# Kernel tuning notes

Hardware: AMD Instinct MI355X
Metric: run time of the kernel (lower is better)

The kernel has to match this reference:

```python
import jax, jax.numpy as jnp
import numpy as np

H = 64  # hidden size (fixed by module)

def _gru_cell(x, h, Wih, Whh, bih, bhh):
    # PyTorch GRU cell: gates ordered (r, z, n)
    gi = x @ Wih.T + bih            # [B, 3H]
    gh = h @ Whh.T + bhh            # [B, 3H]
    ir, iz, inn = jnp.split(gi, 3, axis=-1)
    hr, hz, hn = jnp.split(gh, 3, axis=-1)
    r = jax.nn.sigmoid(ir + hr)
    z = jax.nn.sigmoid(iz + hz)
    n = jnp.tanh(inn + r * hn)
    return (1.0 - z) * n + z * h


def setup_inputs() -> dict:
    key = jax.random.key(0)
    ks = jax.random.split(key, 24)
    B, T, NI = 16384, 256, 6
    s = 1.0 / np.sqrt(H)  # torch default GRU init scale
    f32 = jnp.float32
    u = lambda k, shp: jax.random.uniform(k, shp, dtype=f32, minval=-s, maxval=s)
    inp = {
        "x": jax.random.normal(ks[0], (B, T, NI), dtype=f32),
        "target_len": 180,
        # encoder GRU, layer 0 (input size NI) and layer 1 (input size H)
        "e_Wih0": u(ks[1], (3 * H, NI)), "e_Whh0": u(ks[2], (3 * H, H)),
        "e_bih0": u(ks[3], (3 * H,)),    "e_bhh0": u(ks[4], (3 * H,)),
        "e_Wih1": u(ks[5], (3 * H, H)),  "e_Whh1": u(ks[6], (3 * H, H)),
        "e_bih1": u(ks[7], (3 * H,)),    "e_bhh1": u(ks[8], (3 * H,)),
        # decoder GRU, layer 0 (input size 1) and layer 1 (input size H)
        "d_Wih0": u(ks[9], (3 * H, 1)),  "d_Whh0": u(ks[10], (3 * H, H)),
        "d_bih0": u(ks[11], (3 * H,)),   "d_bhh0": u(ks[12], (3 * H,)),
        "d_Wih1": u(ks[13], (3 * H, H)), "d_Whh1": u(ks[14], (3 * H, H)),
        "d_bih1": u(ks[15], (3 * H,)),   "d_bhh1": u(ks[16], (3 * H,)),
        # heads
        "W_on": u(ks[17], (1, H)), "b_on": u(ks[18], (1,)),
        "W_cv": u(ks[19], (1, H)), "b_cv": u(ks[20], (1,)),
    }
    return inp


def reference(x, target_len,
              e_Wih0, e_Whh0, e_bih0, e_bhh0, e_Wih1, e_Whh1, e_bih1, e_bhh1,
              d_Wih0, d_Whh0, d_bih0, d_bhh0, d_Wih1, d_Whh1, d_bih1, d_bhh1,
              W_on, b_on, W_cv, b_cv):
    B = x.shape[0]
    on_threshold = 0.5

    # ---- encoder: 2-layer GRU over the input sequence, keep final hidden ----
    def enc_step(carry, xt):
        h0, h1 = carry
        h0 = _gru_cell(xt, h0, e_Wih0, e_Whh0, e_bih0, e_bhh0)
        h1 = _gru_cell(h0, h1, e_Wih1, e_Whh1, e_bih1, e_bhh1)
        return (h0, h1), None

    h_init = (jnp.zeros((B, H), x.dtype), jnp.zeros((B, H), x.dtype))
    (h0, h1), _ = jax.lax.scan(enc_step, h_init, jnp.swapaxes(x, 0, 1))  # [T,B,NI]

    def dec_step(carry, _):
        prev, h0, h1 = carry                                   # prev: [B,1]
        h0 = _gru_cell(prev, h0, d_Wih0, d_Whh0, d_bih0, d_bhh0)
        h1 = _gru_cell(h0, h1, d_Wih1, d_Whh1, d_bih1, d_bhh1)
        cv = h1 @ W_cv.T + b_cv                                # [B,1]
        logit = h1 @ W_on.T + b_on                             # [B,1]
        gated = (jax.nn.sigmoid(logit) > on_threshold).astype(cv.dtype) * cv
        return (gated, h0, h1), gated

    prev0 = jnp.zeros((B, 1), x.dtype)
    _, outs = jax.lax.scan(dec_step, (prev0, h0, h1), None, length=target_len)
    # outs: [target_len, B, 1] -> [B, target_len, 1] (torch.cat along dim=1)
    return jnp.swapaxes(outs, 0, 1)
```

## Files before the change

kernel.cpp:

```cpp
#include <hip/hip_runtime.h>
#include <math.h>

#define TENC 256
#define NIE  6
#define LH   68
#define WSTR 68

__shared__ float sW1[192 * WSTR];
__shared__ float sU1[192 * WSTR];
__shared__ float sHd[132];
__shared__ float sh0[64 * LH];
__shared__ float sh1[64 * LH];

__device__ __forceinline__ float sigm_(float x) { return 1.0f / (1.0f + expf(-x)); }

__device__ __forceinline__ void fma4(float& acc, const float4& a, const float4& b) {
    acc = fmaf(a.x, b.x, acc);
    acc = fmaf(a.y, b.y, acc);
    acc = fmaf(a.z, b.z, acc);
    acc = fmaf(a.w, b.w, acc);
}

__device__ __forceinline__ void stage_w1(const float* __restrict__ W1,
                                         const float* __restrict__ U1) {
    for (int s = threadIdx.x; s < 12288; s += 512) {
        int k = s & 63, row = s >> 6;
        int g = row >> 6, j = row & 63;
        int d = (j * 3 + g) * WSTR + k;
        sW1[d] = W1[s];
        sU1[d] = U1[s];
    }
}

template<int KIN>
__device__ __forceinline__ void layer0_c(const float* __restrict__ U0,
                                         const float* w0r, const float* w0z,
                                         const float* w0n,
                                         const float* xin,
                                         const float* b_r, const float* b_z,
                                         const float* b_nx, const float* b_nh,
                                         int jB, int bl, float hn[2][4])
{
    float ar[2][4], az[2][4], anx[2][4], anh[2][4];
#pragma unroll
    for (int g = 0; g < 4; ++g) {
#pragma unroll
        for (int jj = 0; jj < 2; ++jj) {
            ar[jj][g] = b_r[jj]; az[jj][g] = b_z[jj];
            anx[jj][g] = b_nx[jj]; anh[jj][g] = b_nh[jj];
        }
    }
#pragma unroll
    for (int jj = 0; jj < 2; ++jj)
#pragma unroll
        for (int g = 0; g < 4; ++g)
#pragma unroll
            for (int k = 0; k < KIN; ++k) {
                ar[jj][g]  = fmaf(w0r[jj * KIN + k], xin[g * KIN + k], ar[jj][g]);
                az[jj][g]  = fmaf(w0z[jj * KIN + k], xin[g * KIN + k], az[jj][g]);
                anx[jj][g] = fmaf(w0n[jj * KIN + k], xin[g * KIN + k], anx[jj][g]);
            }
    const float* u0 = U0 + (size_t)jB * 64;
    const float* u1 = U0 + (size_t)(jB + 1) * 64;
    const float* hr0 = sh0 + bl * LH;
#pragma unroll 2
    for (int kc = 0; kc < 64; kc += 4) {
        float4 hv[4];
#pragma unroll
        for (int g = 0; g < 4; ++g)
            hv[g] = *(const float4*)(hr0 + g * (16 * LH) + kc);
        float4 r0 = *(const float4*)(u0 + kc);
        float4 z0 = *(const float4*)(u0 + 4096 + kc);
        float4 n0 = *(const float4*)(u0 + 8192 + kc);
        float4 r1 = *(const float4*)(u1 + kc);
        float4 z1 = *(const float4*)(u1 + 4096 + kc);
        float4 n1 = *(const float4*)(u1 + 8192 + kc);
#pragma unroll
        for (int g = 0; g < 4; ++g) {
            fma4(ar[0][g], r0, hv[g]); fma4(az[0][g], z0, hv[g]); fma4(anh[0][g], n0, hv[g]);
            fma4(ar[1][g], r1, hv[g]); fma4(az[1][g], z1, hv[g]); fma4(anh[1][g], n1, hv[g]);
        }
    }
#pragma unroll
    for (int g = 0; g < 4; ++g) {
        float2 ho = *(const float2*)(sh0 + (bl + 16 * g) * LH + jB);
        float hold[2] = {ho.x, ho.y};
#pragma unroll
        for (int jj = 0; jj < 2; ++jj) {
            float r = sigm_(ar[jj][g]);
            float z = sigm_(az[jj][g]);
            float n = tanhf(fmaf(r, anh[jj][g], anx[jj][g]));
            hn[jj][g] = fmaf(z, hold[jj] - n, n);
        }
    }
}

__device__ __forceinline__ void layer1_c(const float* b_r, const float* b_z,
                                         const float* b_nx, const float* b_nh,
                                         int jB, int bl, float hn[2][4])
{
    float ar[2][4], az[2][4], anx[2][4], anh[2][4];
#pragma unroll
    for (int g = 0; g < 4; ++g) {
#pragma unroll
        for (int jj = 0; jj < 2; ++jj) {
            ar[jj][g] = b_r[jj]; az[jj][g] = b_z[jj];
            anx[jj][g] = b_nx[jj]; anh[jj][g] = b_nh[jj];
        }
    }
    const float* wb0 = sW1 + (jB * 3) * WSTR;
    const float* wb1 = sW1 + ((jB + 1) * 3) * WSTR;
    const float* ub0 = sU1 + (jB * 3) * WSTR;
    const float* ub1 = sU1 + ((jB + 1) * 3) * WSTR;
    const float* xr0 = sh0 + bl * LH;
    const float* hr0 = sh1 + bl * LH;
#pragma unroll 2
    for (int kc = 0; kc < 64; kc += 4) {
        float4 xv[4], hv[4];
#pragma unroll
        for (int g = 0; g < 4; ++g) {
            xv[g] = *(const float4*)(xr0 + g * (16 * LH) + kc);
            hv[g] = *(const float4*)(hr0 + g * (16 * LH) + kc);
        }
        float4 wr0 = *(const float4*)(wb0 + kc);
        float4 wz0 = *(const float4*)(wb0 + WSTR + kc);
        float4 wn0 = *(const float4*)(wb0 + 2 * WSTR + kc);
        float4 ur0 = *(const float4*)(ub0 + kc);
        float4 uz0 = *(const float4*)(ub0 + WSTR + kc);
        float4 un0 = *(const float4*)(ub0 + 2 * WSTR + kc);
        float4 wr1 = *(const float4*)(wb1 + kc);
        float4 wz1 = *(const float4*)(wb1 + WSTR + kc);
        float4 wn1 = *(const float4*)(wb1 + 2 * WSTR + kc);
        float4 ur1 = *(const float4*)(ub1 + kc);
        float4 uz1 = *(const float4*)(ub1 + WSTR + kc);
        float4 un1 = *(const float4*)(ub1 + 2 * WSTR + kc);
#pragma unroll
        for (int g = 0; g < 4; ++g) {
            fma4(ar[0][g], wr0, xv[g]);  fma4(ar[0][g], ur0, hv[g]);
            fma4(az[0][g], wz0, xv[g]);  fma4(az[0][g], uz0, hv[g]);
            fma4(anx[0][g], wn0, xv[g]); fma4(anh[0][g], un0, hv[g]);
            fma4(ar[1][g], wr1, xv[g]);  fma4(ar[1][g], ur1, hv[g]);
            fma4(az[1][g], wz1, xv[g]);  fma4(az[1][g], uz1, hv[g]);
            fma4(anx[1][g], wn1, xv[g]); fma4(anh[1][g], un1, hv[g]);
        }
    }
#pragma unroll
    for (int g = 0; g < 4; ++g) {
        float2 ho = *(const float2*)(sh1 + (bl + 16 * g) * LH + jB);
        float hold[2] = {ho.x, ho.y};
#pragma unroll
        for (int jj = 0; jj < 2; ++jj) {
            float r = sigm_(ar[jj][g]);
            float z = sigm_(az[jj][g]);
            float n = tanhf(fmaf(r, anh[jj][g], anx[jj][g]));
            hn[jj][g] = fmaf(z, hold[jj] - n, n);
        }
    }
}

extern "C" __global__ void __launch_bounds__(512, 2)
ccseq_kernel(const float* __restrict__ x, const int* __restrict__ p_tlen,
             const float* __restrict__ eW0, const float* __restrict__ eU0,
             const float* __restrict__ eBi0, const float* __restrict__ eBh0,
             const float* __restrict__ eW1, const float* __restrict__ eU1,
             const float* __restrict__ eBi1, const float* __restrict__ eBh1,
             const float* __restrict__ dW0, const float* __restrict__ dU0,
             const float* __restrict__ dBi0, const float* __restrict__ dBh0,
             const float* __restrict__ dW1, const float* __restrict__ dU1,
             const float* __restrict__ dBi1, const float* __restrict__ dBh1,
             const float* __restrict__ Won, const float* __restrict__ bon,
             const float* __restrict__ Wcv, const float* __restrict__ bcv,
             float* __restrict__ out)
{
    const int tid  = threadIdx.x;
    const int lane = tid & 63;
    const int wv   = tid >> 6;
    const int jg   = lane >> 4;
    const int bl   = lane & 15;
    const int jB   = wv * 8 + jg * 2;
    const int tlen = p_tlen[0];

    if (tid < 64) { sHd[tid] = Wcv[tid]; sHd[64 + tid] = Won[tid]; }
    for (int i = tid; i < 64 * LH; i += 512) { sh0[i] = 0.0f; sh1[i] = 0.0f; }
    stage_w1(eW1, eU1);
    __syncthreads();

    float w0r[2 * NIE], w0z[2 * NIE], w0n[2 * NIE];
#pragma unroll
    for (int jj = 0; jj < 2; ++jj)
#pragma unroll
        for (int k = 0; k < NIE; ++k) {
            w0r[jj * NIE + k] = eW0[(jB + jj) * NIE + k];
            w0z[jj * NIE + k] = eW0[(64 + jB + jj) * NIE + k];
            w0n[jj * NIE + k] = eW0[(128 + jB + jj) * NIE + k];
        }
    float eb_r[2], eb_z[2], eb_nx[2], eb_nh[2];
    float e1_r[2], e1_z[2], e1_nx[2], e1_nh[2];
#pragma unroll
    for (int jj = 0; jj < 2; ++jj) {
        int j = jB + jj;
        eb_r[jj]  = eBi0[j] + eBh0[j];
        eb_z[jj]  = eBi0[64 + j] + eBh0[64 + j];
        eb_nx[jj] = eBi0[128 + j];
        eb_nh[jj] = eBh0[128 + j];
        e1_r[jj]  = eBi1[j] + eBh1[j];
        e1_z[jj]  = eBi1[64 + j] + eBh1[64 + j];
        e1_nx[jj] = eBi1[128 + j];
        e1_nh[jj] = eBh1[128 + j];
    }

    const size_t bstr = (size_t)TENC * NIE;
    const float* xb[4];
#pragma unroll
    for (int g = 0; g < 4; ++g)
        xb[g] = x + (size_t)(blockIdx.x * 64 + bl + 16 * g) * bstr;

    float xc[4 * NIE], xn[4 * NIE];
#pragma unroll
    for (int g = 0; g < 4; ++g)
#pragma unroll
        for (int k = 0; k < NIE; ++k) xc[g * NIE + k] = xb[g][k];

    for (int t = 0; t < TENC; ++t) {
        const int tn = (t + 1 < TENC) ? (t + 1) : t;
#pragma unroll
        for (int g = 0; g < 4; ++g)
#pragma unroll
            for (int k = 0; k < NIE; ++k) xn[g * NIE + k] = xb[g][tn * NIE + k];

        float hn[2][4];
        layer0_c<NIE>(eU0, w0r, w0z, w0n, xc, eb_r, eb_z, eb_nx, eb_nh, jB, bl, hn);
        __syncthreads();
#pragma unroll
        for (int g = 0; g < 4; ++g)
            *(float2*)(sh0 + (bl + 16 * g) * LH + jB) = make_float2(hn[0][g], hn[1][g]);
        __syncthreads();

        layer1_c(e1_r, e1_z, e1_nx, e1_nh, jB, bl, hn);
        __syncthreads();
#pragma unroll
        for (int g = 0; g < 4; ++g)
            *(float2*)(sh1 + (bl + 16 * g) * LH + jB) = make_float2(hn[0][g], hn[1][g]);
        __syncthreads();

#pragma unroll
        for (int i = 0; i < 4 * NIE; ++i) xc[i] = xn[i];
    }

    stage_w1(dW1, dU1);
    float v0r[2], v0z[2], v0n[2];
    float db_r[2], db_z[2], db_nx[2], db_nh[2];
    float d1_r[2], d1_z[2], d1_nx[2], d1_nh[2];
#pragma unroll
    for (int jj = 0; jj < 2; ++jj) {
        int j = jB + jj;
        v0r[jj] = dW0[j]; v0z[jj] = dW0[64 + j]; v0n[jj] = dW0[128 + j];
        db_r[jj]  = dBi0[j] + dBh0[j];
        db_z[jj]  = dBi0[64 + j] + dBh0[64 + j];
        db_nx[jj] = dBi0[128 + j];
        db_nh[jj] = dBh0[128 + j];
        d1_r[jj]  = dBi1[j] + dBh1[j];
        d1_z[jj]  = dBi1[64 + j] + dBh1[64 + j];
        d1_nx[jj] = dBi1[128 + j];
        d1_nh[jj] = dBh1[128 + j];
    }
    const float hbc = bcv[0], hbo = bon[0];
    __syncthreads();

    float prev[4] = {0.0f, 0.0f, 0.0f, 0.0f};
    for (int t = 0; t < tlen; ++t) {
        float hn[2][4];
        layer0_c<1>(dU0, v0r, v0z, v0n, prev, db_r, db_z, db_nx, db_nh, jB, bl, hn);
        __syncthreads();
#pragma unroll
        for (int g = 0; g < 4; ++g)
            *(float2*)(sh0 + (bl + 16 * g) * LH + jB) = make_float2(hn[0][g], hn[1][g]);
        __syncthreads();

        layer1_c(d1_r, d1_z, d1_nx, d1_nh, jB, bl, hn);
        __syncthreads();
#pragma unroll
        for (int g = 0; g < 4; ++g)
            *(float2*)(sh1 + (bl + 16 * g) * LH + jB) = make_float2(hn[0][g], hn[1][g]);
        __syncthreads();

        float cv[4] = {hbc, hbc, hbc, hbc};
        float lg[4] = {hbo, hbo, hbo, hbo};
        const float* hr0 = sh1 + bl * LH;
#pragma unroll 2
        for (int kc = 0; kc < 64; kc += 4) {
            float4 wc = *(const float4*)(sHd + kc);
            float4 wo = *(const float4*)(sHd + 64 + kc);
#pragma unroll
            for (int g = 0; g < 4; ++g) {
                float4 h4 = *(const float4*)(hr0 + g * (16 * LH) + kc);
                fma4(cv[g], wc, h4);
                fma4(lg[g], wo, h4);
            }
        }
#pragma unroll
        for (int g = 0; g < 4; ++g)
            prev[g] = (lg[g] > 0.0f) ? cv[g] : 0.0f;
        if (tid < 16) {
#pragma unroll
            for (int g = 0; g < 4; ++g)
                out[(size_t)(blockIdx.x * 64 + bl + 16 * g) * tlen + t] = prev[g];
        }
    }
}

extern "C" void kernel_launch(void* const* d_in, const int* in_sizes, int n_in,
                              void* d_out, int out_size, void* d_ws, size_t ws_size,
                              hipStream_t stream)
{
    (void)n_in; (void)out_size; (void)d_ws; (void)ws_size;
    const float* x    = (const float*)d_in[0];
    const int*   tl   = (const int*)d_in[1];
    const float* eW0  = (const float*)d_in[2];
    const float* eU0  = (const float*)d_in[3];
    const float* eBi0 = (const float*)d_in[4];
    const float* eBh0 = (const float*)d_in[5];
    const float* eW1  = (const float*)d_in[6];
    const float* eU1  = (const float*)d_in[7];
    const float* eBi1 = (const float*)d_in[8];
    const float* eBh1 = (const float*)d_in[9];
    const float* dW0  = (const float*)d_in[10];
    const float* dU0  = (const float*)d_in[11];
    const float* dBi0 = (const float*)d_in[12];
    const float* dBh0 = (const float*)d_in[13];
    const float* dW1  = (const float*)d_in[14];
    const float* dU1  = (const float*)d_in[15];
    const float* dBi1 = (const float*)d_in[16];
    const float* dBh1 = (const float*)d_in[17];
    const float* Won  = (const float*)d_in[18];
    const float* bon  = (const float*)d_in[19];
    const float* Wcv  = (const float*)d_in[20];
    const float* bcv  = (const float*)d_in[21];

    const int B    = in_sizes[0] / (TENC * NIE);
    const int nblk = B / 64;

    ccseq_kernel<<<dim3(nblk), dim3(512), 0, stream>>>(
        x, tl, eW0, eU0, eBi0, eBh0, eW1, eU1, eBi1, eBh1,
        dW0, dU0, dBi0, dBh0, dW1, dU1, dBi1, dBh1,
        Won, bon, Wcv, bcv, (float*)d_out);
}
```

Measured before the change: 9.694 ms.

## Double-buffer hidden states to halve barriers and read W1 from global

Hidden states are ping-ponged between two LDS buffers per layer, so new values are written straight to the other buffer and each layer update needs one barrier instead of two. The layer-1 input weights are read from global memory (cache) instead of LDS, which frees shared memory for the extra buffers. Encoder input loads are also vectorized into float2 reads. The trade-off is more global/cache weight traffic in the inner layer-1 loop and more LDS spent on buffers.

New measurement: 10.26 ms. 1.06x slower.

```diff
diff --git a/kernel.cpp b/kernel.cpp
--- a/kernel.cpp
+++ b/kernel.cpp
@@ -6,11 +6,10 @@
 #define LH   68
 #define WSTR 68
 
-__shared__ float sW1[192 * WSTR];
 __shared__ float sU1[192 * WSTR];
 __shared__ float sHd[132];
-__shared__ float sh0[64 * LH];
-__shared__ float sh1[64 * LH];
+__shared__ float sh0a[64 * LH], sh0b[64 * LH];
+__shared__ float sh1a[64 * LH], sh1b[64 * LH];
 
 __device__ __forceinline__ float sigm_(float x) { return 1.0f / (1.0f + expf(-x)); }
 
@@ -21,14 +20,11 @@
     acc = fmaf(a.w, b.w, acc);
 }
 
-__device__ __forceinline__ void stage_w1(const float* __restrict__ W1,
-                                         const float* __restrict__ U1) {
+__device__ __forceinline__ void stage_u1(const float* __restrict__ U1) {
     for (int s = threadIdx.x; s < 12288; s += 512) {
         int k = s & 63, row = s >> 6;
         int g = row >> 6, j = row & 63;
-        int d = (j * 3 + g) * WSTR + k;
-        sW1[d] = W1[s];
-        sU1[d] = U1[s];
+        sU1[(j * 3 + g) * WSTR + k] = U1[s];
     }
 }
 
@@ -39,17 +35,17 @@
                                          const float* xin,
                                          const float* b_r, const float* b_z,
                                          const float* b_nx, const float* b_nh,
+                                         const float* __restrict__ h0r,
                                          int jB, int bl, float hn[2][4])
 {
     float ar[2][4], az[2][4], anx[2][4], anh[2][4];
 #pragma unroll
-    for (int g = 0; g < 4; ++g) {
+    for (int g = 0; g < 4; ++g)
 #pragma unroll
         for (int jj = 0; jj < 2; ++jj) {
             ar[jj][g] = b_r[jj]; az[jj][g] = b_z[jj];
             anx[jj][g] = b_nx[jj]; anh[jj][g] = b_nh[jj];
         }
-    }
 #pragma unroll
     for (int jj = 0; jj < 2; ++jj)
 #pragma unroll
@@ -62,7 +58,7 @@
             }
     const float* u0 = U0 + (size_t)jB * 64;
     const float* u1 = U0 + (size_t)(jB + 1) * 64;
-    const float* hr0 = sh0 + bl * LH;
+    const float* hr0 = h0r + bl * LH;
 #pragma unroll 2
     for (int kc = 0; kc < 64; kc += 4) {
         float4 hv[4];
@@ -83,7 +79,7 @@
     }
 #pragma unroll
     for (int g = 0; g < 4; ++g) {
-        float2 ho = *(const float2*)(sh0 + (bl + 16 * g) * LH + jB);
+        float2 ho = *(const float2*)(h0r + (bl + 16 * g) * LH + jB);
         float hold[2] = {ho.x, ho.y};
 #pragma unroll
         for (int jj = 0; jj < 2; ++jj) {
@@ -95,42 +91,43 @@
     }
 }
 
-__device__ __forceinline__ void layer1_c(const float* b_r, const float* b_z,
+__device__ __forceinline__ void layer1_c(const float* __restrict__ W1,
+                                         const float* b_r, const float* b_z,
                                          const float* b_nx, const float* b_nh,
+                                         const float* __restrict__ x0r,
+                                         const float* __restrict__ h1r,
                                          int jB, int bl, float hn[2][4])
 {
     float ar[2][4], az[2][4], anx[2][4], anh[2][4];
 #pragma unroll
-    for (int g = 0; g < 4; ++g) {
+    for (int g = 0; g < 4; ++g)
 #pragma unroll
         for (int jj = 0; jj < 2; ++jj) {
             ar[jj][g] = b_r[jj]; az[jj][g] = b_z[jj];
             anx[jj][g] = b_nx[jj]; anh[jj][g] = b_nh[jj];
         }
-    }
-    const float* wb0 = sW1 + (jB * 3) * WSTR;
-    const float* wb1 = sW1 + ((jB + 1) * 3) * WSTR;
+    const float* wp = W1 + (size_t)jB * 64;
     const float* ub0 = sU1 + (jB * 3) * WSTR;
     const float* ub1 = sU1 + ((jB + 1) * 3) * WSTR;
-    const float* xr0 = sh0 + bl * LH;
-    const float* hr0 = sh1 + bl * LH;
+    const float* xr0 = x0r + bl * LH;
+    const float* hr0 = h1r + bl * LH;
 #pragma unroll 2
     for (int kc = 0; kc < 64; kc += 4) {
+        float4 wr0 = *(const float4*)(wp + kc);
+        float4 wz0 = *(const float4*)(wp + 4096 + kc);
+        float4 wn0 = *(const float4*)(wp + 8192 + kc);
+        float4 wr1 = *(const float4*)(wp + 64 + kc);
+        float4 wz1 = *(const float4*)(wp + 4160 + kc);
+        float4 wn1 = *(const float4*)(wp + 8256 + kc);
         float4 xv[4], hv[4];
 #pragma unroll
         for (int g = 0; g < 4; ++g) {
             xv[g] = *(const float4*)(xr0 + g * (16 * LH) + kc);
             hv[g] = *(const float4*)(hr0 + g * (16 * LH) + kc);
         }
-        float4 wr0 = *(const float4*)(wb0 + kc);
-        float4 wz0 = *(const float4*)(wb0 + WSTR + kc);
-        float4 wn0 = *(const float4*)(wb0 + 2 * WSTR + kc);
         float4 ur0 = *(const float4*)(ub0 + kc);
         float4 uz0 = *(const float4*)(ub0 + WSTR + kc);
         float4 un0 = *(const float4*)(ub0 + 2 * WSTR + kc);
-        float4 wr1 = *(const float4*)(wb1 + kc);
-        float4 wz1 = *(const float4*)(wb1 + WSTR + kc);
-        float4 wn1 = *(const float4*)(wb1 + 2 * WSTR + kc);
         float4 ur1 = *(const float4*)(ub1 + kc);
         float4 uz1 = *(const float4*)(ub1 + WSTR + kc);
         float4 un1 = *(const float4*)(ub1 + 2 * WSTR + kc);
@@ -146,7 +143,7 @@
     }
 #pragma unroll
     for (int g = 0; g < 4; ++g) {
-        float2 ho = *(const float2*)(sh1 + (bl + 16 * g) * LH + jB);
+        float2 ho = *(const float2*)(h1r + (bl + 16 * g) * LH + jB);
         float hold[2] = {ho.x, ho.y};
 #pragma unroll
         for (int jj = 0; jj < 2; ++jj) {
@@ -181,9 +178,14 @@
     const int tlen = p_tlen[0];
 
     if (tid < 64) { sHd[tid] = Wcv[tid]; sHd[64 + tid] = Won[tid]; }
-    for (int i = tid; i < 64 * LH; i += 512) { sh0[i] = 0.0f; sh1[i] = 0.0f; }
-    stage_w1(eW1, eU1);
+    for (int i = tid; i < 64 * LH; i += 512) {
+        sh0a[i] = 0.0f; sh0b[i] = 0.0f; sh1a[i] = 0.0f; sh1b[i] = 0.0f;
+    }
+    stage_u1(eU1);
     __syncthreads();
+
+    float* r0 = sh0a; float* w0 = sh0b;
+    float* r1 = sh1a; float* w1 = sh1b;
 
     float w0r[2 * NIE], w0z[2 * NIE], w0n[2 * NIE];
 #pragma unroll
@@ -217,37 +219,47 @@
 
     float xc[4 * NIE], xn[4 * NIE];
 #pragma unroll
-    for (int g = 0; g < 4; ++g)
-#pragma unroll
-        for (int k = 0; k < NIE; ++k) xc[g * NIE + k] = xb[g][k];
+    for (int g = 0; g < 4; ++g) {
+        float2 p0 = *(const float2*)(xb[g]);
+        float2 p1 = *(const float2*)(xb[g] + 2);
+        float2 p2 = *(const float2*)(xb[g] + 4);
+        xc[g * NIE + 0] = p0.x; xc[g * NIE + 1] = p0.y;
+        xc[g * NIE + 2] = p1.x; xc[g * NIE + 3] = p1.y;
+        xc[g * NIE + 4] = p2.x; xc[g * NIE + 5] = p2.y;
+    }
 
     for (int t = 0; t < TENC; ++t) {
         const int tn = (t + 1 < TENC) ? (t + 1) : t;
 #pragma unroll
-        for (int g = 0; g < 4; ++g)
-#pragma unroll
-            for (int k = 0; k < NIE; ++k) xn[g * NIE + k] = xb[g][tn * NIE + k];
+        for (int g = 0; g < 4; ++g) {
+            float2 p0 = *(const float2*)(xb[g] + tn * NIE);
+            float2 p1 = *(const float2*)(xb[g] + tn * NIE + 2);
+            float2 p2 = *(const float2*)(xb[g] + tn * NIE + 4);
+            xn[g * NIE + 0] = p0.x; xn[g * NIE + 1] = p0.y;
+            xn[g * NIE + 2] = p1.x; xn[g * NIE + 3] = p1.y;
+            xn[g * NIE + 4] = p2.x; xn[g * NIE + 5] = p2.y;
+        }
 
         float hn[2][4];
-        layer0_c<NIE>(eU0, w0r, w0z, w0n, xc, eb_r, eb_z, eb_nx, eb_nh, jB, bl, hn);
+        layer0_c<NIE>(eU0, w0r, w0z, w0n, xc, eb_r, eb_z, eb_nx, eb_nh, r0, jB, bl, hn);
+#pragma unroll
+        for (int g = 0; g < 4; ++g)
+            *(float2*)(w0 + (bl + 16 * g) * LH + jB) = make_float2(hn[0][g], hn[1][g]);
         __syncthreads();
-#pragma unroll
-        for (int g = 0; g < 4; ++g)
-            *(float2*)(sh0 + (bl + 16 * g) * LH + jB) = make_float2(hn[0][g], hn[1][g]);
+
+        layer1_c(eW1, e1_r, e1_z, e1_nx, e1_nh, w0, r1, jB, bl, hn);
+#pragma unroll
+        for (int g = 0; g < 4; ++g)
+            *(float2*)(w1 + (bl + 16 * g) * LH + jB) = make_float2(hn[0][g], hn[1][g]);
         __syncthreads();
 
-        layer1_c(e1_r, e1_z, e1_nx, e1_nh, jB, bl, hn);
-        __syncthreads();
-#pragma unroll
-        for (int g = 0; g < 4; ++g)
-            *(float2*)(sh1 + (bl + 16 * g) * LH + jB) = make_float2(hn[0][g], hn[1][g]);
-        __syncthreads();
-
+        { float* tp = r0; r0 = w0; w0 = tp; }
+        { float* tp = r1; r1 = w1; w1 = tp; }
 #pragma unroll
         for (int i = 0; i < 4 * NIE; ++i) xc[i] = xn[i];
     }
 
-    stage_w1(dW1, dU1);
+    stage_u1(dU1);
     float v0r[2], v0z[2], v0n[2];
     float db_r[2], db_z[2], db_nx[2], db_nh[2];
     float d1_r[2], d1_z[2], d1_nx[2], d1_nh[2];
@@ -270,23 +282,21 @@
     float prev[4] = {0.0f, 0.0f, 0.0f, 0.0f};
     for (int t = 0; t < tlen; ++t) {
         float hn[2][4];
-        layer0_c<1>(dU0, v0r, v0z, v0n, prev, db_r, db_z, db_nx, db_nh, jB, bl, hn);
+        layer0_c<1>(dU0, v0r, v0z, v0n, prev, db_r, db_z, db_nx, db_nh, r0, jB, bl, hn);
+#pragma unroll
+        for (int g = 0; g < 4; ++g)
+            *(float2*)(w0 + (bl + 16 * g) * LH + jB) = make_float2(hn[0][g], hn[1][g]);
         __syncthreads();
-#pragma unroll
-        for (int g = 0; g < 4; ++g)
-            *(float2*)(sh0 + (bl + 16 * g) * LH + jB) = make_float2(hn[0][g], hn[1][g]);
-        __syncthreads();
-
-        layer1_c(d1_r, d1_z, d1_nx, d1_nh, jB, bl, hn);
-        __syncthreads();
-#pragma unroll
-        for (int g = 0; g < 4; ++g)
-            *(float2*)(sh1 + (bl + 16 * g) * LH + jB) = make_float2(hn[0][g], hn[1][g]);
+
+        layer1_c(dW1, d1_r, d1_z, d1_nx, d1_nh, w0, r1, jB, bl, hn);
+#pragma unroll
+        for (int g = 0; g < 4; ++g)
+            *(float2*)(w1 + (bl + 16 * g) * LH + jB) = make_float2(hn[0][g], hn[1][g]);
         __syncthreads();
 
         float cv[4] = {hbc, hbc, hbc, hbc};
         float lg[4] = {hbo, hbo, hbo, hbo};
-        const float* hr0 = sh1 + bl * LH;
+        const float* hr0 = w1 + bl * LH;
 #pragma unroll 2
         for (int kc = 0; kc < 64; kc += 4) {
             float4 wc = *(const float4*)(sHd + kc);
@@ -306,6 +316,9 @@
             for (int g = 0; g < 4; ++g)
                 out[(size_t)(blockIdx.x * 64 + bl + 16 * g) * tlen + t] = prev[g];
         }
+
+        { float* tp = r0; r0 = w0; w0 = tp; }
+        { float* tp = r1; r1 = w1; w1 = tp; }
     }
 }
 
```
